# Optimization experiments

Hardware: AMD Instinct MI355X
Metric: run time of the kernel (lower is better)

The kernel has to match this reference:

```python
import jax, jax.numpy as jnp
import numpy as np

B, S, D, H, L, MLP, WIN = 4, 1024, 256, 8, 2, 1024, 64
HD = D // H
NEG = -1e9  # emulates -inf additive mask; exp underflows to exact 0

_idx = jnp.arange(S)
BAND = jnp.where(jnp.abs(_idx[:, None] - _idx[None, :]) <= WIN, 0.0, NEG).astype(jnp.float32)


def setup_inputs() -> dict:
    key = jax.random.key(0)
    ks = iter(jax.random.split(key, 16))
    r = lambda shape, s=0.02: jax.random.normal(next(ks), shape, dtype=jnp.float32) * s
    return {
        "x": jax.random.normal(next(ks), (B, S, D), dtype=jnp.float32),
        "scale": jnp.ones((1,), jnp.float32) * (D ** -0.5),
        "Win_a": r((L, 3 * D, D)), "bin_a": jnp.zeros((L, 3 * D), jnp.float32),
        "Wout_a": r((L, D, D)), "bout_a": jnp.zeros((L, D), jnp.float32),
        "Win_e": r((L, 3 * D, D)), "bin_e": jnp.zeros((L, 3 * D), jnp.float32),
        "Wout_e": r((L, D, D)), "bout_e": jnp.zeros((L, D), jnp.float32),
        "ln1_g": jnp.ones((L, D), jnp.float32), "ln1_b": jnp.zeros((L, D), jnp.float32),
        "ln2_g": jnp.ones((L, D), jnp.float32), "ln2_b": jnp.zeros((L, D), jnp.float32),
        "W1": r((L, MLP, D)), "b1": jnp.zeros((L, MLP), jnp.float32),
        "W2": r((L, D, MLP)), "b2": jnp.zeros((L, D), jnp.float32),
        "lnf_g": jnp.ones((D,), jnp.float32), "lnf_b": jnp.zeros((D,), jnp.float32),
    }


def _layernorm(x, g, b, eps=1e-5):
    m = jnp.mean(x, axis=-1, keepdims=True)
    v = jnp.mean(jnp.square(x - m), axis=-1, keepdims=True)
    return (x - m) * jax.lax.rsqrt(v + eps) * g + b


def _mha(x, Win, bin_, Wout, bout, mask=None):
    # torch nn.MultiheadAttention (batch_first=True), dropout=0
    b, s, _ = x.shape
    qkv = x @ Win.T + bin_                       # (b, s, 3D)
    q, k, v = jnp.split(qkv, 3, axis=-1)
    split = lambda t: t.reshape(b, s, H, HD).transpose(0, 2, 1, 3)  # (b, H, s, HD)
    q, k, v = split(q), split(k), split(v)
    scores = jnp.einsum('bhqd,bhkd->bhqk', q, k) / np.float32(np.sqrt(HD))
    if mask is not None:
        scores = scores + mask
    attn = jax.nn.softmax(scores, axis=-1)
    out = jnp.einsum('bhqk,bhkd->bhqd', attn, v).transpose(0, 2, 1, 3).reshape(b, s, D)
    return out @ Wout.T + bout


def reference(x, scale, Win_a, bin_a, Wout_a, bout_a, Win_e, bin_e, Wout_e, bout_e,
              ln1_g, ln1_b, ln2_g, ln2_b, W1, b1, W2, b2, lnf_g, lnf_b):
    # ScaledSinusoidalPositionalEncoding returns arange(S)*scale, shape (S,1)
    pos = jnp.arange(S, dtype=jnp.float32) * scale[0]   # (S,)
    x = x + pos[:, None]                                 # broadcast (B,S,D)+(S,1)
    for l in range(L):
        xi = _mha(x, Win_a[l], bin_a[l], Wout_a[l], bout_a[l])
        x = _layernorm(x + xi, ln1_g[l], ln1_b[l])
        xe = _mha(x, Win_e[l], bin_e[l], Wout_e[l], bout_e[l], mask=BAND)
        attended = _layernorm(x + xe, ln2_g[l], ln2_b[l])
        h = jax.nn.gelu(attended @ W1[l].T + b1[l], approximate=False)
        x = attended + h @ W2[l].T + b2[l]
    return _layernorm(x, lnf_g, lnf_b)
```

## Files before the change

### kernel.cpp

```cpp
#include <hip/hip_runtime.h>
#include <math.h>

#define BB 4
#define SS 1024
#define DD 256
#define HH 8
#define HD 32
#define D3 768
#define MLP 1024
#define NTOK (BB * SS)
#define NSEG 2

typedef __attribute__((ext_vector_type(8))) short short8;
typedef __attribute__((ext_vector_type(4))) float f32x4;

__device__ __forceinline__ unsigned short f2bfu(float f) {
    union { float f; unsigned i; } u; u.f = f;
    unsigned r = u.i + 0x7fffu + ((u.i >> 16) & 1u);
    return (unsigned short)(r >> 16);
}
__device__ __forceinline__ float bfu2f(unsigned short h) {
    union { unsigned i; float f; } u; u.i = ((unsigned)h) << 16; return u.f;
}

#define W_TOT 2097152
#define WL0   196608
__global__ __launch_bounds__(256) void conv_weights(
    const float* __restrict__ a0, const float* __restrict__ a1,
    const float* __restrict__ a2, const float* __restrict__ a3,
    const float* __restrict__ a4, const float* __restrict__ a5,
    unsigned short* __restrict__ out, unsigned short* __restrict__ out_lo)
{
    int i = blockIdx.x * 256 + threadIdx.x;
    const float* s; int off;
    if      (i <  393216) { s = a0; off = 0;       }
    else if (i <  524288) { s = a1; off = 393216;  }
    else if (i <  917504) { s = a2; off = 524288;  }
    else if (i < 1048576) { s = a3; off = 917504;  }
    else if (i < 1572864) { s = a4; off = 1048576; }
    else                  { s = a5; off = 1572864; }
    float v = s[i - off];
    unsigned short h = f2bfu(v);
    out[i] = h;
    if (i < WL0) out_lo[i] = f2bfu(v - bfu2f(h));
}

__global__ __launch_bounds__(256) void add_pos_kernel(
    const float* __restrict__ x, const float* __restrict__ scale,
    float* __restrict__ out, unsigned short* __restrict__ outh,
    unsigned short* __restrict__ outl, int n)
{
    int i = blockIdx.x * 256 + threadIdx.x;
    if (i >= n) return;
    int s = (i >> 8) & (SS - 1);
    float v = x[i] + (float)s * scale[0];
    out[i] = v;
    unsigned short h = f2bfu(v);
    outh[i] = h;
    outl[i] = f2bfu(v - bfu2f(h));
}

#define LDP 40
__global__ __launch_bounds__(256) void gemm_mfma(
    const unsigned short* __restrict__ A, const unsigned short* __restrict__ W,
    const float* __restrict__ bias, const float* __restrict__ resid,
    float* __restrict__ outf, unsigned short* __restrict__ outb,
    int M, int N, int K, int act)
{
    __shared__ __align__(16) unsigned short As[64 * LDP];
    __shared__ __align__(16) unsigned short Bs[128 * LDP];
    const int t = threadIdx.x;
    const int lane = t & 63, wave = t >> 6;
    const int wr = wave >> 1, wc = wave & 1;
    const int m0 = blockIdx.y * 64, n0 = blockIdx.x * 128;
    const int sr = t >> 2;
    const int sc = (t & 3) * 8;

    const unsigned short* Ag = A + (size_t)(m0 + sr) * K + sc;
    const unsigned short* Wg = W + (size_t)(n0 + sr) * K + sc;

    f32x4 acc[2][4];
    #pragma unroll
    for (int i = 0; i < 2; i++)
        #pragma unroll
        for (int j = 0; j < 4; j++)
            acc[i][j] = (f32x4){0.f, 0.f, 0.f, 0.f};

    const int lm = lane & 15, lk = (lane >> 4) * 8;

    for (int k0 = 0; k0 < K; k0 += 32) {
        uint4 a0 = *(const uint4*)(Ag + k0);
        uint4 b0 = *(const uint4*)(Wg + k0);
        uint4 b1 = *(const uint4*)(Wg + (size_t)64 * K + k0);
        __syncthreads();
        *(uint4*)&As[sr * LDP + sc]        = a0;
        *(uint4*)&Bs[sr * LDP + sc]        = b0;
        *(uint4*)&Bs[(sr + 64) * LDP + sc] = b1;
        __syncthreads();

        short8 af[2], bf[4];
        #pragma unroll
        for (int i = 0; i < 2; i++)
            af[i] = *(const short8*)&As[(wr * 32 + i * 16 + lm) * LDP + lk];
        #pragma unroll
        for (int j = 0; j < 4; j++)
            bf[j] = *(const short8*)&Bs[(wc * 64 + j * 16 + lm) * LDP + lk];
        #pragma unroll
        for (int i = 0; i < 2; i++)
            #pragma unroll
            for (int j = 0; j < 4; j++)
                acc[i][j] = __builtin_amdgcn_mfma_f32_16x16x32_bf16(
                    af[i], bf[j], acc[i][j], 0, 0, 0);
    }

    const int lq = lane >> 4;
    #pragma unroll
    for (int j = 0; j < 4; j++) {
        int col = n0 + wc * 64 + j * 16 + lm;
        float bv = bias[col];
        #pragma unroll
        for (int i = 0; i < 2; i++) {
            #pragma unroll
            for (int r = 0; r < 4; r++) {
                int row = m0 + wr * 32 + i * 16 + lq * 4 + r;
                float v = acc[i][j][r] + bv;
                if (act) v = 0.5f * v * (1.0f + erff(v * 0.70710678118654752f));
                size_t idx = (size_t)row * N + col;
                if (resid) v += resid[idx];
                if (outf) outf[idx] = v;
                if (outb) outb[idx] = f2bfu(v);
            }
        }
    }
}

__global__ __launch_bounds__(256) void gemm_mfma_split(
    const unsigned short* __restrict__ Ah, const unsigned short* __restrict__ Al,
    const unsigned short* __restrict__ Wh, const unsigned short* __restrict__ Wl,
    const float* __restrict__ bias,
    unsigned short* __restrict__ outh, unsigned short* __restrict__ outl,
    int M, int N, int K)
{
    __shared__ __align__(16) unsigned short Ash[64 * LDP];
    __shared__ __align__(16) unsigned short Asl[64 * LDP];
    __shared__ __align__(16) unsigned short Bsh[128 * LDP];
    __shared__ __align__(16) unsigned short Bsl[128 * LDP];
    const int t = threadIdx.x;
    const int lane = t & 63, wave = t >> 6;
    const int wr = wave >> 1, wc = wave & 1;
    const int m0 = blockIdx.y * 64, n0 = blockIdx.x * 128;
    const int sr = t >> 2;
    const int sc = (t & 3) * 8;

    const size_t oA = (size_t)(m0 + sr) * K + sc;
    const size_t oW = (size_t)(n0 + sr) * K + sc;

    f32x4 acc[2][4];
    #pragma unroll
    for (int i = 0; i < 2; i++)
        #pragma unroll
        for (int j = 0; j < 4; j++)
            acc[i][j] = (f32x4){0.f, 0.f, 0.f, 0.f};

    const int lm = lane & 15, lk = (lane >> 4) * 8;

    for (int k0 = 0; k0 < K; k0 += 32) {
        uint4 ah0 = *(const uint4*)(Ah + oA + k0);
        uint4 al0 = *(const uint4*)(Al + oA + k0);
        uint4 bh0 = *(const uint4*)(Wh + oW + k0);
        uint4 bh1 = *(const uint4*)(Wh + oW + (size_t)64 * K + k0);
        uint4 bl0 = *(const uint4*)(Wl + oW + k0);
        uint4 bl1 = *(const uint4*)(Wl + oW + (size_t)64 * K + k0);
        __syncthreads();
        *(uint4*)&Ash[sr * LDP + sc]        = ah0;
        *(uint4*)&Asl[sr * LDP + sc]        = al0;
        *(uint4*)&Bsh[sr * LDP + sc]        = bh0;
        *(uint4*)&Bsh[(sr + 64) * LDP + sc] = bh1;
        *(uint4*)&Bsl[sr * LDP + sc]        = bl0;
        *(uint4*)&Bsl[(sr + 64) * LDP + sc] = bl1;
        __syncthreads();

        short8 afh[2], afl[2], bfh[4], bfl[4];
        #pragma unroll
        for (int i = 0; i < 2; i++) {
            afh[i] = *(const short8*)&Ash[(wr * 32 + i * 16 + lm) * LDP + lk];
            afl[i] = *(const short8*)&Asl[(wr * 32 + i * 16 + lm) * LDP + lk];
        }
        #pragma unroll
        for (int j = 0; j < 4; j++) {
            bfh[j] = *(const short8*)&Bsh[(wc * 64 + j * 16 + lm) * LDP + lk];
            bfl[j] = *(const short8*)&Bsl[(wc * 64 + j * 16 + lm) * LDP + lk];
        }
        #pragma unroll
        for (int i = 0; i < 2; i++)
            #pragma unroll
            for (int j = 0; j < 4; j++) {
                acc[i][j] = __builtin_amdgcn_mfma_f32_16x16x32_bf16(
                    afl[i], bfh[j], acc[i][j], 0, 0, 0);
                acc[i][j] = __builtin_amdgcn_mfma_f32_16x16x32_bf16(
                    afh[i], bfl[j], acc[i][j], 0, 0, 0);
                acc[i][j] = __builtin_amdgcn_mfma_f32_16x16x32_bf16(
                    afh[i], bfh[j], acc[i][j], 0, 0, 0);
            }
    }

    const int lq = lane >> 4;
    #pragma unroll
    for (int j = 0; j < 4; j++) {
        int col = n0 + wc * 64 + j * 16 + lm;
        float bv = bias[col];
        #pragma unroll
        for (int i = 0; i < 2; i++) {
            #pragma unroll
            for (int r = 0; r < 4; r++) {
                int row = m0 + wr * 32 + i * 16 + lq * 4 + r;
                float v = acc[i][j][r] + bv;
                size_t idx = (size_t)row * N + col;
                unsigned short h = f2bfu(v);
                outh[idx] = h;
                outl[idx] = f2bfu(v - bfu2f(h));
            }
        }
    }
}

template<bool SPLIT>
__global__ __launch_bounds__(256) void attn_mfma(
    const unsigned short* __restrict__ qkvh,
    const unsigned short* __restrict__ qkvl,
    unsigned short* __restrict__ outb,
    float* __restrict__ Of, float2* __restrict__ Ml,
    int win, int nseg)
{
    __shared__ __align__(16) unsigned short Ks [64 * 40];
    __shared__ __align__(16) unsigned short Vt [32 * 72];
    __shared__ __align__(16) unsigned short Ps [64 * 72];
    __shared__ __align__(16) unsigned short Ksl[SPLIT ? 64 * 40 : 8];
    __shared__ __align__(16) unsigned short Vtl[SPLIT ? 32 * 72 : 8];

    const int t = threadIdx.x;
    const int wave = t >> 6, lane = t & 63;
    const int lm = lane & 15, quad = lane >> 4;
    const int i0 = blockIdx.x * 64, h = blockIdx.y;
    const int z = blockIdx.z;
    const int b = z / nseg, seg = z - b * nseg;
    const int sr = t >> 2, sc8 = (t & 3) * 8;

    const size_t qoff = ((size_t)(b * SS) + i0 + 16 * wave + lm) * D3 + h * HD + quad * 8;
    short8 qh = *(const short8*)(qkvh + qoff);
    short8 ql = {};
    if constexpr (SPLIT) ql = *(const short8*)(qkvl + qoff);

    float m[4], l[4];
    f32x4 o[2];
    #pragma unroll
    for (int r = 0; r < 4; r++) { m[r] = -1e30f; l[r] = 0.f; }
    o[0] = (f32x4){0.f, 0.f, 0.f, 0.f};
    o[1] = (f32x4){0.f, 0.f, 0.f, 0.f};

    int t0 = 0, t1 = SS / 64 - 1;
    const bool masked = (win < SS);
    if (masked) {
        t0 = (i0 - win) >> 6;        if (t0 < 0) t0 = 0;
        t1 = (i0 + 63 + win) >> 6;   if (t1 > SS / 64 - 1) t1 = SS / 64 - 1;
    }
    const int per = (t1 - t0 + nseg) / nseg;
    const int s0 = t0 + seg * per;
    const int s1 = (s0 + per - 1 < t1) ? (s0 + per - 1) : t1;
    const float scl = 0.17677669529663688f;

    for (int kt = s0; kt <= s1; kt++) {
        const int k0 = kt * 64;
        __syncthreads();
        {
            const size_t koff = ((size_t)(b * SS) + k0 + sr) * D3 + DD + h * HD + sc8;
            short8 kv = *(const short8*)(qkvh + koff);
            *(short8*)&Ks[sr * 40 + sc8] = kv;
            short8 vv = *(const short8*)(qkvh + koff + DD);
            #pragma unroll
            for (int c = 0; c < 8; c++)
                Vt[(sc8 + c) * 72 + sr] = ((unsigned short*)&vv)[c];
            if constexpr (SPLIT) {
                short8 kl = *(const short8*)(qkvl + koff);
                *(short8*)&Ksl[sr * 40 + sc8] = kl;
                short8 vl = *(const short8*)(qkvl + koff + DD);
                #pragma unroll
                for (int c = 0; c < 8; c++)
                    Vtl[(sc8 + c) * 72 + sr] = ((unsigned short*)&vl)[c];
            }
        }
        __syncthreads();

        f32x4 s[4];
        #pragma unroll
        for (int cb = 0; cb < 4; cb++) {
            short8 kf = *(const short8*)&Ks[(16 * cb + lm) * 40 + quad * 8];
            f32x4 a = (f32x4){0.f, 0.f, 0.f, 0.f};
            if constexpr (SPLIT) {
                short8 kfl = *(const short8*)&Ksl[(16 * cb + lm) * 40 + quad * 8];
                a = __builtin_amdgcn_mfma_f32_16x16x32_bf16(ql, kf,  a, 0, 0, 0);
                a = __builtin_amdgcn_mfma_f32_16x16x32_bf16(qh, kfl, a, 0, 0, 0);
            }
            a = __builtin_amdgcn_mfma_f32_16x16x32_bf16(qh, kf, a, 0, 0, 0);
            s[cb] = a;
        }

        float sc[4][4];
        #pragma unroll
        for (int cb = 0; cb < 4; cb++)
            #pragma unroll
            for (int r = 0; r < 4; r++) {
                float v = s[cb][r] * scl;
                if (masked) {
                    int di = (i0 + 16 * wave + quad * 4 + r) - (k0 + 16 * cb + lm);
                    if (di > win || di < -win) v = -1e30f;
                }
                sc[cb][r] = v;
            }

        #pragma unroll
        for (int r = 0; r < 4; r++) {
            float tm = fmaxf(fmaxf(sc[0][r], sc[1][r]), fmaxf(sc[2][r], sc[3][r]));
            tm = fmaxf(tm, __shfl_xor(tm, 1, 64));
            tm = fmaxf(tm, __shfl_xor(tm, 2, 64));
            tm = fmaxf(tm, __shfl_xor(tm, 4, 64));
            tm = fmaxf(tm, __shfl_xor(tm, 8, 64));
            float mn = fmaxf(m[r], tm);
            float alpha = __expf(m[r] - mn);
            float p0 = __expf(sc[0][r] - mn), p1 = __expf(sc[1][r] - mn);
            float p2 = __expf(sc[2][r] - mn), p3 = __expf(sc[3][r] - mn);
            float ps = p0 + p1 + p2 + p3;
            ps += __shfl_xor(ps, 1, 64);
            ps += __shfl_xor(ps, 2, 64);
            ps += __shfl_xor(ps, 4, 64);
            ps += __shfl_xor(ps, 8, 64);
            l[r] = l[r] * alpha + ps;
            o[0][r] *= alpha;
            o[1][r] *= alpha;
            m[r] = mn;
            const int pr = (16 * wave + quad * 4 + r) * 72 + lm;
            Ps[pr +  0] = f2bfu(p0);
            Ps[pr + 16] = f2bfu(p1);
            Ps[pr + 32] = f2bfu(p2);
            Ps[pr + 48] = f2bfu(p3);
        }

        #pragma unroll
        for (int kc = 0; kc < 2; kc++) {
            short8 pf = *(const short8*)&Ps[(16 * wave + lm) * 72 + 32 * kc + quad * 8];
            #pragma unroll
            for (int nh = 0; nh < 2; nh++) {
                short8 vf = *(const short8*)&Vt[(16 * nh + lm) * 72 + 32 * kc + quad * 8];
                o[nh] = __builtin_amdgcn_mfma_f32_16x16x32_bf16(pf, vf, o[nh], 0, 0, 0);
                if constexpr (SPLIT) {
                    short8 vfl = *(const short8*)&Vtl[(16 * nh + lm) * 72 + 32 * kc + quad * 8];
                    o[nh] = __builtin_amdgcn_mfma_f32_16x16x32_bf16(pf, vfl, o[nh], 0, 0, 0);
                }
            }
        }
    }

    if (nseg == 1) {
        #pragma unroll
        for (int r = 0; r < 4; r++) {
            float invl = 1.0f / l[r];
            size_t base = ((size_t)(b * SS) + i0 + 16 * wave + quad * 4 + r) * DD + h * HD + lm;
            outb[base]      = f2bfu(o[0][r] * invl);
            outb[base + 16] = f2bfu(o[1][r] * invl);
        }
    } else {
        #pragma unroll
        for (int r = 0; r < 4; r++) {
            int row = i0 + 16 * wave + quad * 4 + r;
            size_t base = ((size_t)(seg * NTOK) + b * SS + row) * DD + h * HD + lm;
            Of[base]      = o[0][r];
            Of[base + 16] = o[1][r];
            if (lm == 0)
                Ml[((size_t)(seg * NTOK) + b * SS + row) * HH + h] =
                    make_float2(m[r], l[r]);
        }
    }
}

__global__ __launch_bounds__(256) void attn_combine(
    const float* __restrict__ Of, const float2* __restrict__ Ml,
    unsigned short* __restrict__ out)
{
    int i = blockIdx.x * 256 + threadIdx.x;
    int token = i >> 8;
    int h = (i & 255) >> 5;
    float2 a = Ml[(size_t)token * HH + h];
    float2 c = Ml[((size_t)NTOK + token) * HH + h];
    float M = fmaxf(a.x, c.x);
    float w0 = __expf(a.x - M), w1 = __expf(c.x - M);
    float ov = Of[i] * w0 + Of[(size_t)NTOK * DD + i] * w1;
    float lv = a.y * w0 + c.y * w1;
    out[i] = f2bfu(ov / lv);
}

__global__ __launch_bounds__(256) void ln_kernel(
    const float* __restrict__ a, const float* __restrict__ r,
    const float* __restrict__ g, const float* __restrict__ bt,
    float* __restrict__ outf, unsigned short* __restrict__ outb)
{
    const int wave = threadIdx.x >> 6, lane = threadIdx.x & 63;
    const int row = blockIdx.x * 4 + wave;
    const size_t base = (size_t)row * DD + lane * 4;
    float4 v = *(const float4*)(a + base);
    if (r) {
        float4 rv = *(const float4*)(r + base);
        v.x += rv.x; v.y += rv.y; v.z += rv.z; v.w += rv.w;
    }
    float s = v.x + v.y + v.z + v.w;
    #pragma unroll
    for (int off = 1; off < 64; off <<= 1) s += __shfl_xor(s, off, 64);
    float mean = s * (1.0f / 256.0f);
    float4 dv = { v.x - mean, v.y - mean, v.z - mean, v.w - mean };
    float s2 = dv.x * dv.x + dv.y * dv.y + dv.z * dv.z + dv.w * dv.w;
    #pragma unroll
    for (int off = 1; off < 64; off <<= 1) s2 += __shfl_xor(s2, off, 64);
    float rst = rsqrtf(s2 * (1.0f / 256.0f) + 1e-5f);
    float4 g4 = *(const float4*)(g + lane * 4);
    float4 b4 = *(const float4*)(bt + lane * 4);
    float4 ov = { dv.x * rst * g4.x + b4.x, dv.y * rst * g4.y + b4.y,
                  dv.z * rst * g4.z + b4.z, dv.w * rst * g4.w + b4.w };
    if (outf) *(float4*)(outf + base) = ov;
    if (outb) {
        ushort4 u = { f2bfu(ov.x), f2bfu(ov.y), f2bfu(ov.z), f2bfu(ov.w) };
        *(ushort4*)(outb + base) = u;
    }
}

extern "C" void kernel_launch(void* const* d_in, const int* in_sizes, int n_in,
                              void* d_out, int out_size, void* d_ws, size_t ws_size,
                              hipStream_t stream)
{
    const float* xin   = (const float*)d_in[0];
    const float* scale = (const float*)d_in[1];
    const float* Win_a = (const float*)d_in[2];
    const float* bin_a = (const float*)d_in[3];
    const float* Wout_a= (const float*)d_in[4];
    const float* bout_a= (const float*)d_in[5];
    const float* Win_e = (const float*)d_in[6];
    const float* bin_e = (const float*)d_in[7];
    const float* Wout_e= (const float*)d_in[8];
    const float* bout_e= (const float*)d_in[9];
    const float* ln1_g = (const float*)d_in[10];
    const float* ln1_b = (const float*)d_in[11];
    const float* ln2_g = (const float*)d_in[12];
    const float* ln2_b = (const float*)d_in[13];
    const float* W1    = (const float*)d_in[14];
    const float* b1    = (const float*)d_in[15];
    const float* W2    = (const float*)d_in[16];
    const float* b2    = (const float*)d_in[17];
    const float* lnf_g = (const float*)d_in[18];
    const float* lnf_b = (const float*)d_in[19];

    char* ws = (char*)d_ws;
    float* X    = (float*)ws;                     ws += (size_t)NTOK * DD * 4;
    float* X2   = (float*)ws;                     ws += (size_t)NTOK * DD * 4;
    float* P    = (float*)ws;                     ws += (size_t)NTOK * DD * 4;
    unsigned short* Xb   = (unsigned short*)ws;   ws += (size_t)NTOK * DD * 2;
    unsigned short* Xlb  = (unsigned short*)ws;   ws += (size_t)NTOK * DD * 2;
    unsigned short* X2b  = (unsigned short*)ws;   ws += (size_t)NTOK * DD * 2;
    unsigned short* ATb  = (unsigned short*)ws;   ws += (size_t)NTOK * DD * 2;
    unsigned short* QKVb = (unsigned short*)ws;   ws += (size_t)NTOK * D3 * 2;
    unsigned short* QKVl = (unsigned short*)ws;   ws += (size_t)NTOK * D3 * 2;
    unsigned short* HMLb = (unsigned short*)ws;   ws += (size_t)NTOK * MLP * 2;
    unsigned short* Wb   = (unsigned short*)ws;   ws += (size_t)W_TOT * 2;
    unsigned short* Wl0  = (unsigned short*)ws;   ws += (size_t)WL0 * 2;
    float2* Ml           = (float2*)ws;           ws += (size_t)NSEG * NTOK * HH * 8;

    float* Of = (float*)HMLb;

    unsigned short* WinA_b  = Wb + 0;
    unsigned short* WoutA_b = Wb + 393216;
    unsigned short* WinE_b  = Wb + 524288;
    unsigned short* WoutE_b = Wb + 917504;
    unsigned short* W1_b    = Wb + 1048576;
    unsigned short* W2_b    = Wb + 1572864;

    conv_weights<<<W_TOT / 256, 256, 0, stream>>>(
        Win_a, Wout_a, Win_e, Wout_e, W1, W2, Wb, Wl0);
    add_pos_kernel<<<(NTOK * DD + 255) / 256, 256, 0, stream>>>(
        xin, scale, X, Xb, Xlb, NTOK * DD);

    float* cur = X;            float* oth = X2;
    unsigned short* curb = Xb; unsigned short* othb = X2b;

    for (int l = 0; l < 2; l++) {
        if (l == 0) {
            gemm_mfma_split<<<dim3(D3 / 128, NTOK / 64), 256, 0, stream>>>(
                Xb, Xlb, WinA_b, Wl0, bin_a, QKVb, QKVl, NTOK, D3, DD);
            attn_mfma<true><<<dim3(SS / 64, HH, BB * NSEG), 256, 0, stream>>>(
                QKVb, QKVl, nullptr, Of, Ml, 1 << 28, NSEG);
        } else {
            gemm_mfma<<<dim3(D3 / 128, NTOK / 64), 256, 0, stream>>>(
                curb, WinA_b + (size_t)l * D3 * DD, bin_a + (size_t)l * D3,
                nullptr, nullptr, QKVb, NTOK, D3, DD, 0);
            attn_mfma<false><<<dim3(SS / 64, HH, BB * NSEG), 256, 0, stream>>>(
                QKVb, nullptr, nullptr, Of, Ml, 1 << 28, NSEG);
        }
        attn_combine<<<NTOK * DD / 256, 256, 0, stream>>>(Of, Ml, ATb);
        gemm_mfma<<<dim3(DD / 128, NTOK / 64), 256, 0, stream>>>(
            ATb, WoutA_b + (size_t)l * DD * DD, bout_a + (size_t)l * DD,
            nullptr, P, nullptr, NTOK, DD, DD, 0);
        ln_kernel<<<NTOK / 4, 256, 0, stream>>>(
            P, cur, ln1_g + l * DD, ln1_b + l * DD, oth, othb);

        gemm_mfma<<<dim3(D3 / 128, NTOK / 64), 256, 0, stream>>>(
            othb, WinE_b + (size_t)l * D3 * DD, bin_e + (size_t)l * D3,
            nullptr, nullptr, QKVb, NTOK, D3, DD, 0);
        attn_mfma<false><<<dim3(SS / 64, HH, BB), 256, 0, stream>>>(
            QKVb, nullptr, ATb, nullptr, nullptr, 64, 1);
        gemm_mfma<<<dim3(DD / 128, NTOK / 64), 256, 0, stream>>>(
            ATb, WoutE_b + (size_t)l * DD * DD, bout_e + (size_t)l * DD,
            nullptr, P, nullptr, NTOK, DD, DD, 0);
        ln_kernel<<<NTOK / 4, 256, 0, stream>>>(
            P, oth, ln2_g + l * DD, ln2_b + l * DD, cur, curb);

        gemm_mfma<<<dim3(MLP / 128, NTOK / 64), 256, 0, stream>>>(
            curb, W1_b + (size_t)l * MLP * DD, b1 + (size_t)l * MLP,
            nullptr, nullptr, HMLb, NTOK, MLP, DD, 1);
        gemm_mfma<<<dim3(DD / 128, NTOK / 64), 256, 0, stream>>>(
            HMLb, W2_b + (size_t)l * DD * MLP, b2 + (size_t)l * DD,
            cur, oth, othb, NTOK, DD, MLP, 0);

        float* tf = cur; cur = oth; oth = tf;
        unsigned short* tb = curb; curb = othb; othb = tb;
    }

    ln_kernel<<<NTOK / 4, 256, 0, stream>>>(cur, nullptr, lnf_g, lnf_b,
                                            (float*)d_out, nullptr);
}
```

Measured before the change: 364.8 us.

## Write V transposed from QKV GEMM and read K/V directly in attention

The QKV projection epilogue now scatters the V third into a per-(batch, head) transposed layout. The attention kernel drops its shared-memory K/V staging and barriers and loads MFMA fragments for K and V straight from global memory. The full-attention path uses four key segments instead of two, stores partial outputs as bf16, and the combine kernel is generalised to NSEG segments. This removes LDS transposes and syncs and raises parallelism, at the cost of uncoalesced scattered V stores, redundant global K/V reads across waves, and lower precision in the partial outputs.

```diff
diff --git a/kernel.cpp b/kernel.cpp
--- a/kernel.cpp
+++ b/kernel.cpp
@@ -9,7 +9,7 @@
 #define D3 768
 #define MLP 1024
 #define NTOK (BB * SS)
-#define NSEG 2
+#define NSEG 4
 
 typedef __attribute__((ext_vector_type(8))) short short8;
 typedef __attribute__((ext_vector_type(4))) float f32x4;
@@ -60,11 +60,18 @@
     outl[i] = f2bfu(v - bfu2f(h));
 }
 
+__device__ __forceinline__ size_t vt_index(int row, int col512) {
+    int b = row >> 10, s = row & (SS - 1);
+    int h = col512 >> 5, d = col512 & (HD - 1);
+    return (((size_t)b * HH + h) * HD + d) * SS + s;
+}
+
 #define LDP 40
 __global__ __launch_bounds__(256) void gemm_mfma(
     const unsigned short* __restrict__ A, const unsigned short* __restrict__ W,
     const float* __restrict__ bias, const float* __restrict__ resid,
     float* __restrict__ outf, unsigned short* __restrict__ outb,
+    unsigned short* __restrict__ vth,
     int M, int N, int K, int act)
 {
     __shared__ __align__(16) unsigned short As[64 * LDP];
@@ -125,10 +132,14 @@
                 int row = m0 + wr * 32 + i * 16 + lq * 4 + r;
                 float v = acc[i][j][r] + bv;
                 if (act) v = 0.5f * v * (1.0f + erff(v * 0.70710678118654752f));
-                size_t idx = (size_t)row * N + col;
-                if (resid) v += resid[idx];
-                if (outf) outf[idx] = v;
-                if (outb) outb[idx] = f2bfu(v);
+                if (vth && col >= 2 * DD) {
+                    vth[vt_index(row, col - 2 * DD)] = f2bfu(v);
+                } else {
+                    size_t idx = (size_t)row * N + col;
+                    if (resid) v += resid[idx];
+                    if (outf) outf[idx] = v;
+                    if (outb) outb[idx] = f2bfu(v);
+                }
             }
         }
     }
@@ -139,6 +150,7 @@
     const unsigned short* __restrict__ Wh, const unsigned short* __restrict__ Wl,
     const float* __restrict__ bias,
     unsigned short* __restrict__ outh, unsigned short* __restrict__ outl,
+    unsigned short* __restrict__ vth, unsigned short* __restrict__ vtl,
     int M, int N, int K)
 {
     __shared__ __align__(16) unsigned short Ash[64 * LDP];
@@ -215,28 +227,31 @@
             for (int r = 0; r < 4; r++) {
                 int row = m0 + wr * 32 + i * 16 + lq * 4 + r;
                 float v = acc[i][j][r] + bv;
-                size_t idx = (size_t)row * N + col;
                 unsigned short h = f2bfu(v);
-                outh[idx] = h;
-                outl[idx] = f2bfu(v - bfu2f(h));
+                unsigned short lo = f2bfu(v - bfu2f(h));
+                if (col >= 2 * DD) {
+                    size_t vi = vt_index(row, col - 2 * DD);
+                    vth[vi] = h; vtl[vi] = lo;
+                } else {
+                    size_t idx = (size_t)row * N + col;
+                    outh[idx] = h; outl[idx] = lo;
+                }
             }
         }
     }
 }
 
 template<bool SPLIT>
-__global__ __launch_bounds__(256) void attn_mfma(
+__global__ __launch_bounds__(256, 8) void attn_mfma(
     const unsigned short* __restrict__ qkvh,
     const unsigned short* __restrict__ qkvl,
+    const unsigned short* __restrict__ vth,
+    const unsigned short* __restrict__ vtl,
     unsigned short* __restrict__ outb,
-    float* __restrict__ Of, float2* __restrict__ Ml,
+    unsigned short* __restrict__ Ofb, float2* __restrict__ Ml,
     int win, int nseg)
 {
-    __shared__ __align__(16) unsigned short Ks [64 * 40];
-    __shared__ __align__(16) unsigned short Vt [32 * 72];
-    __shared__ __align__(16) unsigned short Ps [64 * 72];
-    __shared__ __align__(16) unsigned short Ksl[SPLIT ? 64 * 40 : 8];
-    __shared__ __align__(16) unsigned short Vtl[SPLIT ? 32 * 72 : 8];
+    __shared__ __align__(16) unsigned short Ps[64 * 72];
 
     const int t = threadIdx.x;
     const int wave = t >> 6, lane = t & 63;
@@ -244,12 +259,16 @@
     const int i0 = blockIdx.x * 64, h = blockIdx.y;
     const int z = blockIdx.z;
     const int b = z / nseg, seg = z - b * nseg;
-    const int sr = t >> 2, sc8 = (t & 3) * 8;
 
     const size_t qoff = ((size_t)(b * SS) + i0 + 16 * wave + lm) * D3 + h * HD + quad * 8;
     short8 qh = *(const short8*)(qkvh + qoff);
     short8 ql = {};
     if constexpr (SPLIT) ql = *(const short8*)(qkvl + qoff);
+
+    const unsigned short* Kg = qkvh + (size_t)(b * SS) * D3 + DD + h * HD;
+    const unsigned short* Kl = SPLIT ? qkvl + (size_t)(b * SS) * D3 + DD + h * HD : nullptr;
+    const unsigned short* Vg = vth + (((size_t)b * HH + h) * HD) * SS;
+    const unsigned short* Vl = SPLIT ? vtl + (((size_t)b * HH + h) * HD) * SS : nullptr;
 
     float m[4], l[4];
     f32x4 o[2];
@@ -271,33 +290,14 @@
 
     for (int kt = s0; kt <= s1; kt++) {
         const int k0 = kt * 64;
-        __syncthreads();
-        {
-            const size_t koff = ((size_t)(b * SS) + k0 + sr) * D3 + DD + h * HD + sc8;
-            short8 kv = *(const short8*)(qkvh + koff);
-            *(short8*)&Ks[sr * 40 + sc8] = kv;
-            short8 vv = *(const short8*)(qkvh + koff + DD);
-            #pragma unroll
-            for (int c = 0; c < 8; c++)
-                Vt[(sc8 + c) * 72 + sr] = ((unsigned short*)&vv)[c];
-            if constexpr (SPLIT) {
-                short8 kl = *(const short8*)(qkvl + koff);
-                *(short8*)&Ksl[sr * 40 + sc8] = kl;
-                short8 vl = *(const short8*)(qkvl + koff + DD);
-                #pragma unroll
-                for (int c = 0; c < 8; c++)
-                    Vtl[(sc8 + c) * 72 + sr] = ((unsigned short*)&vl)[c];
-            }
-        }
-        __syncthreads();
 
         f32x4 s[4];
         #pragma unroll
         for (int cb = 0; cb < 4; cb++) {
-            short8 kf = *(const short8*)&Ks[(16 * cb + lm) * 40 + quad * 8];
+            short8 kf = *(const short8*)(Kg + (size_t)(k0 + 16 * cb + lm) * D3 + quad * 8);
             f32x4 a = (f32x4){0.f, 0.f, 0.f, 0.f};
             if constexpr (SPLIT) {
-                short8 kfl = *(const short8*)&Ksl[(16 * cb + lm) * 40 + quad * 8];
+                short8 kfl = *(const short8*)(Kl + (size_t)(k0 + 16 * cb + lm) * D3 + quad * 8);
                 a = __builtin_amdgcn_mfma_f32_16x16x32_bf16(ql, kf,  a, 0, 0, 0);
                 a = __builtin_amdgcn_mfma_f32_16x16x32_bf16(qh, kfl, a, 0, 0, 0);
             }
@@ -350,10 +350,12 @@
             short8 pf = *(const short8*)&Ps[(16 * wave + lm) * 72 + 32 * kc + quad * 8];
             #pragma unroll
             for (int nh = 0; nh < 2; nh++) {
-                short8 vf = *(const short8*)&Vt[(16 * nh + lm) * 72 + 32 * kc + quad * 8];
+                short8 vf = *(const short8*)(Vg + (size_t)(16 * nh + lm) * SS
+                                             + k0 + 32 * kc + quad * 8);
                 o[nh] = __builtin_amdgcn_mfma_f32_16x16x32_bf16(pf, vf, o[nh], 0, 0, 0);
                 if constexpr (SPLIT) {
-                    short8 vfl = *(const short8*)&Vtl[(16 * nh + lm) * 72 + 32 * kc + quad * 8];
+                    short8 vfl = *(const short8*)(Vl + (size_t)(16 * nh + lm) * SS
+                                                  + k0 + 32 * kc + quad * 8);
                     o[nh] = __builtin_amdgcn_mfma_f32_16x16x32_bf16(pf, vfl, o[nh], 0, 0, 0);
                 }
             }
@@ -372,29 +374,37 @@
         #pragma unroll
         for (int r = 0; r < 4; r++) {
             int row = i0 + 16 * wave + quad * 4 + r;
-            size_t base = ((size_t)(seg * NTOK) + b * SS + row) * DD + h * HD + lm;
-            Of[base]      = o[0][r];
-            Of[base + 16] = o[1][r];
+            size_t base = ((size_t)seg * NTOK + b * SS + row) * DD + h * HD + lm;
+            Ofb[base]      = f2bfu(o[0][r]);
+            Ofb[base + 16] = f2bfu(o[1][r]);
             if (lm == 0)
-                Ml[((size_t)(seg * NTOK) + b * SS + row) * HH + h] =
+                Ml[((size_t)seg * NTOK + b * SS + row) * HH + h] =
                     make_float2(m[r], l[r]);
         }
     }
 }
 
 __global__ __launch_bounds__(256) void attn_combine(
-    const float* __restrict__ Of, const float2* __restrict__ Ml,
+    const unsigned short* __restrict__ Ofb, const float2* __restrict__ Ml,
     unsigned short* __restrict__ out)
 {
     int i = blockIdx.x * 256 + threadIdx.x;
     int token = i >> 8;
     int h = (i & 255) >> 5;
-    float2 a = Ml[(size_t)token * HH + h];
-    float2 c = Ml[((size_t)NTOK + token) * HH + h];
-    float M = fmaxf(a.x, c.x);
-    float w0 = __expf(a.x - M), w1 = __expf(c.x - M);
-    float ov = Of[i] * w0 + Of[(size_t)NTOK * DD + i] * w1;
-    float lv = a.y * w0 + c.y * w1;
+    float2 ml[NSEG];
+    float M = -1e30f;
+    #pragma unroll
+    for (int s = 0; s < NSEG; s++) {
+        ml[s] = Ml[((size_t)s * NTOK + token) * HH + h];
+        M = fmaxf(M, ml[s].x);
+    }
+    float ov = 0.f, lv = 0.f;
+    #pragma unroll
+    for (int s = 0; s < NSEG; s++) {
+        float w = __expf(ml[s].x - M);
+        ov += bfu2f(Ofb[(size_t)s * NTOK * DD + i]) * w;
+        lv += ml[s].y * w;
+    }
     out[i] = f2bfu(ov / lv);
 }
 
@@ -466,12 +476,14 @@
     unsigned short* ATb  = (unsigned short*)ws;   ws += (size_t)NTOK * DD * 2;
     unsigned short* QKVb = (unsigned short*)ws;   ws += (size_t)NTOK * D3 * 2;
     unsigned short* QKVl = (unsigned short*)ws;   ws += (size_t)NTOK * D3 * 2;
+    unsigned short* VTh  = (unsigned short*)ws;   ws += (size_t)NTOK * DD * 2;
+    unsigned short* VTl  = (unsigned short*)ws;   ws += (size_t)NTOK * DD * 2;
     unsigned short* HMLb = (unsigned short*)ws;   ws += (size_t)NTOK * MLP * 2;
     unsigned short* Wb   = (unsigned short*)ws;   ws += (size_t)W_TOT * 2;
     unsigned short* Wl0  = (unsigned short*)ws;   ws += (size_t)WL0 * 2;
     float2* Ml           = (float2*)ws;           ws += (size_t)NSEG * NTOK * HH * 8;
 
-    float* Of = (float*)HMLb;
+    unsigned short* Ofb = HMLb;
 
     unsigned short* WinA_b  = Wb + 0;
     unsigned short* WoutA_b = Wb + 393216;
@@ -491,40 +503,40 @@
     for (int l = 0; l < 2; l++) {
         if (l == 0) {
             gemm_mfma_split<<<dim3(D3 / 128, NTOK / 64), 256, 0, stream>>>(
-                Xb, Xlb, WinA_b, Wl0, bin_a, QKVb, QKVl, NTOK, D3, DD);
+                Xb, Xlb, WinA_b, Wl0, bin_a, QKVb, QKVl, VTh, VTl, NTOK, D3, DD);
             attn_mfma<true><<<dim3(SS / 64, HH, BB * NSEG), 256, 0, stream>>>(
-                QKVb, QKVl, nullptr, Of, Ml, 1 << 28, NSEG);
+                QKVb, QKVl, VTh, VTl, nullptr, Ofb, Ml, 1 << 28, NSEG);
         } else {
             gemm_mfma<<<dim3(D3 / 128, NTOK / 64), 256, 0, stream>>>(
                 curb, WinA_b + (size_t)l * D3 * DD, bin_a + (size_t)l * D3,
-                nullptr, nullptr, QKVb, NTOK, D3, DD, 0);
+                nullptr, nullptr, QKVb, VTh, NTOK, D3, DD, 0);
             attn_mfma<false><<<dim3(SS / 64, HH, BB * NSEG), 256, 0, stream>>>(
-                QKVb, nullptr, nullptr, Of, Ml, 1 << 28, NSEG);
-        }
-        attn_combine<<<NTOK * DD / 256, 256, 0, stream>>>(Of, Ml, ATb);
+                QKVb, nullptr, VTh, nullptr, nullptr, Ofb, Ml, 1 << 28, NSEG);
+        }
+        attn_combine<<<NTOK * DD / 256, 256, 0, stream>>>(Ofb, Ml, ATb);
         gemm_mfma<<<dim3(DD / 128, NTOK / 64), 256, 0, stream>>>(
             ATb, WoutA_b + (size_t)l * DD * DD, bout_a + (size_t)l * DD,
-            nullptr, P, nullptr, NTOK, DD, DD, 0);
+            nullptr, P, nullptr, nullptr, NTOK, DD, DD, 0);
         ln_kernel<<<NTOK / 4, 256, 0, stream>>>(
             P, cur, ln1_g + l * DD, ln1_b + l * DD, oth, othb);
 
         gemm_mfma<<<dim3(D3 / 128, NTOK / 64), 256, 0, stream>>>(
             othb, WinE_b + (size_t)l * D3 * DD, bin_e + (size_t)l * D3,
-            nullptr, nullptr, QKVb, NTOK, D3, DD, 0);
+            nullptr, nullptr, QKVb, VTh, NTOK, D3, DD, 0);
         attn_mfma<false><<<dim3(SS / 64, HH, BB), 256, 0, stream>>>(
-            QKVb, nullptr, ATb, nullptr, nullptr, 64, 1);
+            QKVb, nullptr, VTh, nullptr, ATb, nullptr, nullptr, 64, 1);
         gemm_mfma<<<dim3(DD / 128, NTOK / 64), 256, 0, stream>>>(
             ATb, WoutE_b + (size_t)l * DD * DD, bout_e + (size_t)l * DD,
-            nullptr, P, nullptr, NTOK, DD, DD, 0);
+            nullptr, P, nullptr, nullptr, NTOK, DD, DD, 0);
         ln_kernel<<<NTOK / 4, 256, 0, stream>>>(
             P, oth, ln2_g + l * DD, ln2_b + l * DD, cur, curb);
 
         gemm_mfma<<<dim3(MLP / 128, NTOK / 64), 256, 0, stream>>>(
             curb, W1_b + (size_t)l * MLP * DD, b1 + (size_t)l * MLP,
-            nullptr, nullptr, HMLb, NTOK, MLP, DD, 1);
+            nullptr, nullptr, HMLb, nullptr, NTOK, MLP, DD, 1);
         gemm_mfma<<<dim3(DD / 128, NTOK / 64), 256, 0, stream>>>(
             HMLb, W2_b + (size_t)l * DD * MLP, b2 + (size_t)l * DD,
-            cur, oth, othb, NTOK, DD, MLP, 0);
+            cur, oth, othb, nullptr, NTOK, DD, MLP, 0);
 
         float* tf = cur; cur = oth; oth = tf;
         unsigned short* tb = curb; curb = othb; othb = tb;
```

Result: slower. 460.5 us (+26.2%).
